# Optimization experiments

Measured on AMD Instinct MI355X. Metric: run time of the kernel, lower is better.

## Reference

```python
import jax, jax.numpy as jnp
import numpy as np

EPS = 1e-8
NEG_FILL = -9e15


def _normalize(x):
    # matches torch cosine_similarity's norm clamp with eps=1e-8
    n = jnp.sqrt(jnp.sum(x * x, axis=-1, keepdims=True))
    return x / jnp.maximum(n, EPS)


def setup_inputs() -> dict:
    key = jax.random.key(0)
    k1, k2 = jax.random.split(key)
    N, D = 8192, 512
    cxr_feats = jax.random.normal(k1, (N, D), dtype=jnp.float32)
    ehr_feats = jax.random.normal(k2, (N, D), dtype=jnp.float32)
    temperature = jnp.asarray(0.07, dtype=jnp.float32)
    return {"cxr_feats": cxr_feats, "ehr_feats": ehr_feats, "temperature": temperature}


def reference(cxr_feats, ehr_feats, temperature):
    # normalize then GEMM instead of broadcasted [N,N,D] cosine_similarity
    cn = _normalize(cxr_feats)                      # [N, D]
    en = _normalize(ehr_feats)                      # [N, D]
    cos_sim = jnp.einsum('id,jd->ij', cn, en)       # [N, N]
    cos_sim = cos_sim / temperature
    N = cos_sim.shape[0]
    eye = jnp.eye(N, dtype=bool)
    diag = jnp.diagonal(cos_sim)                    # positives
    cos_neg = jnp.where(eye, NEG_FILL, cos_sim)     # mask self-pairs
    nll_1 = diag - jax.nn.logsumexp(cos_neg, axis=1)
    nll_2 = diag - jax.nn.logsumexp(cos_neg, axis=0)
    loss = -jnp.mean(nll_1 + nll_2)
    return loss
```

## Files before the change

### kernel.cpp

```cpp
#include <hip/hip_runtime.h>
#include <hip/hip_bf16.h>
#include <stdint.h>
#include <stddef.h>

#define NROWS 8192
#define DDIM  512
#define TILE  128
#define BK    64
#define NBLK  (NROWS / TILE)

static_assert(NBLK == 64, "bj extraction assumes 64 col-blocks");

typedef short bf16x8 __attribute__((ext_vector_type(8)));
typedef float f32x4  __attribute__((ext_vector_type(4)));

__device__ __forceinline__ void async_copy16(const void* g, void* l) {
    __builtin_amdgcn_global_load_lds(
        (const __attribute__((address_space(1))) uint32_t*)g,
        (__attribute__((address_space(3))) uint32_t*)l,
        16, 0, 0);
}

struct bh4 { __hip_bfloat16 x, y, z, w; };

__global__ __launch_bounds__(256) void prep_kernel(
    const float* __restrict__ CXR, const float* __restrict__ EHR,
    __hip_bfloat16* __restrict__ CN, __hip_bfloat16* __restrict__ EN,
    float* __restrict__ rowsum ,
    float* __restrict__ out)
{
    if (blockIdx.x < 64) {
        rowsum[blockIdx.x * 256 + threadIdx.x] = 0.f;
        if (blockIdx.x == 0 && threadIdx.x == 0) out[0] = 0.f;
    }
    const int half = (blockIdx.x >= 2048);
    const float* X = half ? EHR : CXR;
    __hip_bfloat16* Y = half ? EN : CN;
    const int row  = (blockIdx.x & 2047) * 4 + (threadIdx.x >> 6);
    const int lane = threadIdx.x & 63;
    const float* xr = X + (size_t)row * DDIM;
    float4 v0 = ((const float4*)xr)[lane];
    float4 v1 = ((const float4*)xr)[lane + 64];
    float ss = v0.x*v0.x + v0.y*v0.y + v0.z*v0.z + v0.w*v0.w
             + v1.x*v1.x + v1.y*v1.y + v1.z*v1.z + v1.w*v1.w;
    #pragma unroll
    for (int d = 1; d < 64; d <<= 1) ss += __shfl_xor(ss, d);
    const float sc = 1.0f / fmaxf(sqrtf(ss), 1e-8f);
    __hip_bfloat16* yr = Y + (size_t)row * DDIM;
    bh4 o0 = { __float2bfloat16(v0.x*sc), __float2bfloat16(v0.y*sc),
               __float2bfloat16(v0.z*sc), __float2bfloat16(v0.w*sc) };
    bh4 o1 = { __float2bfloat16(v1.x*sc), __float2bfloat16(v1.y*sc),
               __float2bfloat16(v1.z*sc), __float2bfloat16(v1.w*sc) };
    ((bh4*)yr)[lane]      = o0;
    ((bh4*)yr)[lane + 64] = o1;
}

__global__ __launch_bounds__(256, 2) void gemm_loss_kernel(
    const __hip_bfloat16* __restrict__ A,
    const __hip_bfloat16* __restrict__ B,
    const float* __restrict__ temp_p,
    float* __restrict__ rowsum,
    float* __restrict__ colsum,
    float* __restrict__ diagv)
{
    __shared__ __hip_bfloat16 As[TILE * BK];
    __shared__ __hip_bfloat16 Bs[TILE * BK];

    const int tid  = threadIdx.x;
    const int lane = tid & 63;
    const int wv   = tid >> 6;
    const int wi   = (wv >> 1) * 64;
    const int wj   = (wv & 1) * 64;
    const int lcol = lane & 15;
    const int q    = lane >> 4;

    const int bi = blockIdx.x & (NBLK - 1);
    const int bj = blockIdx.x >> 6;
    const int row0 = bi * TILE;
    const int col0 = bj * TILE;

    const int sr = lane >> 3;
    const int su = (lane & 7) ^ sr;
    const __hip_bfloat16* Ag = A + (size_t)(row0 + wv * 32 + sr) * DDIM + su * 8;
    const __hip_bfloat16* Bg = B + (size_t)(col0 + wv * 32 + sr) * DDIM + su * 8;

    f32x4 acc[4][4] = {};

    for (int k0 = 0; k0 < DDIM; k0 += BK) {
        __syncthreads();
        #pragma unroll
        for (int c = 0; c < 4; ++c) {
            async_copy16(Ag + (size_t)(c * 8) * DDIM + k0, &As[(wv * 32 + c * 8) * BK]);
            async_copy16(Bg + (size_t)(c * 8) * DDIM + k0, &Bs[(wv * 32 + c * 8) * BK]);
        }
        __syncthreads();

        #pragma unroll
        for (int kk = 0; kk < 2; ++kk) {
            bf16x8 af[4], bfr[4];
            const int u = kk * 4 + q;
            #pragma unroll
            for (int mt = 0; mt < 4; ++mt) {
                const int r = wi + mt * 16 + lcol;
                const int s = u ^ (r & 7);
                af[mt] = *(const bf16x8*)&As[r * BK + s * 8];
            }
            #pragma unroll
            for (int nt = 0; nt < 4; ++nt) {
                const int r = wj + nt * 16 + lcol;
                const int s = u ^ (r & 7);
                bfr[nt] = *(const bf16x8*)&Bs[r * BK + s * 8];
            }
            #pragma unroll
            for (int mt = 0; mt < 4; ++mt)
                #pragma unroll
                for (int nt = 0; nt < 4; ++nt)
                    acc[mt][nt] = __builtin_amdgcn_mfma_f32_16x16x32_bf16(
                        af[mt], bfr[nt], acc[mt][nt], 0, 0, 0);
        }
    }

    const float invT = 1.0f / temp_p[0];
    const float M = invT;

    float rs[4][4];
    float cs[4];
    #pragma unroll
    for (int mt = 0; mt < 4; ++mt)
        #pragma unroll
        for (int r = 0; r < 4; ++r) rs[mt][r] = 0.f;
    #pragma unroll
    for (int nt = 0; nt < 4; ++nt) cs[nt] = 0.f;

    #pragma unroll
    for (int mt = 0; mt < 4; ++mt) {
        #pragma unroll
        for (int nt = 0; nt < 4; ++nt) {
            #pragma unroll
            for (int r = 0; r < 4; ++r) {
                const int gi = row0 + wi + mt * 16 + q * 4 + r;
                const int gj = col0 + wj + nt * 16 + lcol;
                const float sv = acc[mt][nt][r] * invT;
                float e;
                if (gi == gj) { diagv[gi] = sv; e = 0.f; }
                else          { e = __expf(sv - M); }
                rs[mt][r] += e;
                cs[nt]    += e;
            }
        }
    }

    #pragma unroll
    for (int d = 1; d < 16; d <<= 1)
        #pragma unroll
        for (int mt = 0; mt < 4; ++mt)
            #pragma unroll
            for (int r = 0; r < 4; ++r)
                rs[mt][r] += __shfl_xor(rs[mt][r], d);

    #pragma unroll
    for (int d = 16; d < 64; d <<= 1)
        #pragma unroll
        for (int nt = 0; nt < 4; ++nt)
            cs[nt] += __shfl_xor(cs[nt], d);

    if (lcol == 0) {
        #pragma unroll
        for (int mt = 0; mt < 4; ++mt)
            #pragma unroll
            for (int r = 0; r < 4; ++r)
                atomicAdd(&rowsum[row0 + wi + mt * 16 + q * 4 + r], rs[mt][r]);
    }
    if (q == 0) {
        #pragma unroll
        for (int nt = 0; nt < 4; ++nt)
            atomicAdd(&colsum[col0 + wj + nt * 16 + lcol], cs[nt]);
    }
}

__global__ __launch_bounds__(256) void finalize_kernel(
    const float* __restrict__ rowsum, const float* __restrict__ colsum,
    const float* __restrict__ diagv,  const float* __restrict__ temp_p,
    float* __restrict__ out)
{
    __shared__ float red[4];
    const float M = 1.0f / temp_p[0];
    const int i = blockIdx.x * 256 + threadIdx.x;
    float s = 2.f * M + logf(rowsum[i]) + logf(colsum[i]) - 2.f * diagv[i];
    #pragma unroll
    for (int d = 1; d < 64; d <<= 1) s += __shfl_xor(s, d);
    if ((threadIdx.x & 63) == 0) red[threadIdx.x >> 6] = s;
    __syncthreads();
    if (threadIdx.x == 0)
        atomicAdd(out, (red[0] + red[1] + red[2] + red[3]) / (float)NROWS);
}

extern "C" void kernel_launch(void* const* d_in, const int* in_sizes, int n_in,
                              void* d_out, int out_size, void* d_ws, size_t ws_size,
                              hipStream_t stream) {
    (void)in_sizes; (void)n_in; (void)out_size; (void)ws_size;
    const float* cxr    = (const float*)d_in[0];
    const float* ehr    = (const float*)d_in[1];
    const float* temp_p = (const float*)d_in[2];
    float* out = (float*)d_out;

    float* rowsum = (float*)d_ws;
    float* colsum = rowsum + NROWS;
    float* diagv  = colsum + NROWS;
    __hip_bfloat16* cn = (__hip_bfloat16*)(diagv + NROWS);
    __hip_bfloat16* en = cn + (size_t)NROWS * DDIM;

    prep_kernel<<<4096, 256, 0, stream>>>(cxr, ehr, cn, en, rowsum, out);
    gemm_loss_kernel<<<NBLK * NBLK, 256, 0, stream>>>(cn, en, temp_p, rowsum, colsum, diagv);
    finalize_kernel<<<NROWS / 256, 256, 0, stream>>>(rowsum, colsum, diagv, temp_p, out);
}
```

Before: 164.5 us.

## Switch normalized features to FP8 and use scaled 16x16x128 MFMA

Normalized rows are quantized to FP8 in the prep kernel instead of bf16, and the GEMM uses the MI355X scaled f8f6f4 MFMA with K=128 per instruction. Operand bytes, LDS footprint and MFMA instruction count are all cut, and the occupancy hint rises to 3 blocks per CU. The risk is lower precision of the cosine similarities, which are then scaled by 1/T and exponentiated, so loss accuracy may degrade.

```diff
diff --git a/kernel.cpp b/kernel.cpp
--- a/kernel.cpp
+++ b/kernel.cpp
@@ -6,13 +6,14 @@
 #define NROWS 8192
 #define DDIM  512
 #define TILE  128
-#define BK    64
+#define BKB   128
 #define NBLK  (NROWS / TILE)
 
 static_assert(NBLK == 64, "bj extraction assumes 64 col-blocks");
 
-typedef short bf16x8 __attribute__((ext_vector_type(8)));
-typedef float f32x4  __attribute__((ext_vector_type(4)));
+typedef int   v4i  __attribute__((ext_vector_type(4)));
+typedef int   v8i  __attribute__((ext_vector_type(8)));
+typedef float f32x4 __attribute__((ext_vector_type(4)));
 
 __device__ __forceinline__ void async_copy16(const void* g, void* l) {
     __builtin_amdgcn_global_load_lds(
@@ -21,11 +22,13 @@
         16, 0, 0);
 }
 
-struct bh4 { __hip_bfloat16 x, y, z, w; };
+__device__ __forceinline__ v8i cat8(v4i lo, v4i hi) {
+    return __builtin_shufflevector(lo, hi, 0, 1, 2, 3, 4, 5, 6, 7);
+}
 
 __global__ __launch_bounds__(256) void prep_kernel(
     const float* __restrict__ CXR, const float* __restrict__ EHR,
-    __hip_bfloat16* __restrict__ CN, __hip_bfloat16* __restrict__ EN,
+    uint32_t* __restrict__ CN8, uint32_t* __restrict__ EN8,
     float* __restrict__ rowsum ,
     float* __restrict__ out)
 {
@@ -35,7 +38,7 @@
     }
     const int half = (blockIdx.x >= 2048);
     const float* X = half ? EHR : CXR;
-    __hip_bfloat16* Y = half ? EN : CN;
+    uint32_t* Y = half ? EN8 : CN8;
     const int row  = (blockIdx.x & 2047) * 4 + (threadIdx.x >> 6);
     const int lane = threadIdx.x & 63;
     const float* xr = X + (size_t)row * DDIM;
@@ -46,25 +49,25 @@
     #pragma unroll
     for (int d = 1; d < 64; d <<= 1) ss += __shfl_xor(ss, d);
     const float sc = 1.0f / fmaxf(sqrtf(ss), 1e-8f);
-    __hip_bfloat16* yr = Y + (size_t)row * DDIM;
-    bh4 o0 = { __float2bfloat16(v0.x*sc), __float2bfloat16(v0.y*sc),
-               __float2bfloat16(v0.z*sc), __float2bfloat16(v0.w*sc) };
-    bh4 o1 = { __float2bfloat16(v1.x*sc), __float2bfloat16(v1.y*sc),
-               __float2bfloat16(v1.z*sc), __float2bfloat16(v1.w*sc) };
-    ((bh4*)yr)[lane]      = o0;
-    ((bh4*)yr)[lane + 64] = o1;
-}
-
-__global__ __launch_bounds__(256, 2) void gemm_loss_kernel(
-    const __hip_bfloat16* __restrict__ A,
-    const __hip_bfloat16* __restrict__ B,
+    uint32_t* yr = Y + (size_t)row * (DDIM / 4);
+    int w0 = __builtin_amdgcn_cvt_pk_fp8_f32(v0.x*sc, v0.y*sc, 0, false);
+    w0     = __builtin_amdgcn_cvt_pk_fp8_f32(v0.z*sc, v0.w*sc, w0, true);
+    int w1 = __builtin_amdgcn_cvt_pk_fp8_f32(v1.x*sc, v1.y*sc, 0, false);
+    w1     = __builtin_amdgcn_cvt_pk_fp8_f32(v1.z*sc, v1.w*sc, w1, true);
+    yr[lane]      = (uint32_t)w0;
+    yr[lane + 64] = (uint32_t)w1;
+}
+
+__global__ __launch_bounds__(256, 3) void gemm_loss_kernel(
+    const uint8_t* __restrict__ A,
+    const uint8_t* __restrict__ B,
     const float* __restrict__ temp_p,
     float* __restrict__ rowsum,
     float* __restrict__ colsum,
     float* __restrict__ diagv)
 {
-    __shared__ __hip_bfloat16 As[TILE * BK];
-    __shared__ __hip_bfloat16 Bs[TILE * BK];
+    __shared__ uint8_t As[TILE * BKB];
+    __shared__ uint8_t Bs[TILE * BKB];
 
     const int tid  = threadIdx.x;
     const int lane = tid & 63;
@@ -81,43 +84,46 @@
 
     const int sr = lane >> 3;
     const int su = (lane & 7) ^ sr;
-    const __hip_bfloat16* Ag = A + (size_t)(row0 + wv * 32 + sr) * DDIM + su * 8;
-    const __hip_bfloat16* Bg = B + (size_t)(col0 + wv * 32 + sr) * DDIM + su * 8;
+    const uint8_t* Ag = A + (size_t)(row0 + wv * 32 + sr) * DDIM + su * 16;
+    const uint8_t* Bg = B + (size_t)(col0 + wv * 32 + sr) * DDIM + su * 16;
 
     f32x4 acc[4][4] = {};
 
-    for (int k0 = 0; k0 < DDIM; k0 += BK) {
+    for (int k0 = 0; k0 < DDIM; k0 += BKB) {
         __syncthreads();
         #pragma unroll
         for (int c = 0; c < 4; ++c) {
-            async_copy16(Ag + (size_t)(c * 8) * DDIM + k0, &As[(wv * 32 + c * 8) * BK]);
-            async_copy16(Bg + (size_t)(c * 8) * DDIM + k0, &Bs[(wv * 32 + c * 8) * BK]);
+            async_copy16(Ag + (size_t)(c * 8) * DDIM + k0, &As[(wv * 32 + c * 8) * BKB]);
+            async_copy16(Bg + (size_t)(c * 8) * DDIM + k0, &Bs[(wv * 32 + c * 8) * BKB]);
         }
         __syncthreads();
 
-        #pragma unroll
-        for (int kk = 0; kk < 2; ++kk) {
-            bf16x8 af[4], bfr[4];
-            const int u = kk * 4 + q;
-            #pragma unroll
-            for (int mt = 0; mt < 4; ++mt) {
-                const int r = wi + mt * 16 + lcol;
-                const int s = u ^ (r & 7);
-                af[mt] = *(const bf16x8*)&As[r * BK + s * 8];
-            }
-            #pragma unroll
-            for (int nt = 0; nt < 4; ++nt) {
-                const int r = wj + nt * 16 + lcol;
-                const int s = u ^ (r & 7);
-                bfr[nt] = *(const bf16x8*)&Bs[r * BK + s * 8];
-            }
-            #pragma unroll
-            for (int mt = 0; mt < 4; ++mt)
-                #pragma unroll
-                for (int nt = 0; nt < 4; ++nt)
-                    acc[mt][nt] = __builtin_amdgcn_mfma_f32_16x16x32_bf16(
-                        af[mt], bfr[nt], acc[mt][nt], 0, 0, 0);
-        }
+        v8i af[4], bfr[4];
+        #pragma unroll
+        for (int mt = 0; mt < 4; ++mt) {
+            const int r = wi + mt * 16 + lcol;
+            const int rx = r & 7;
+            v4i lo = *(const v4i*)&As[r * BKB + ((2 * q) ^ rx) * 16];
+            v4i hi = *(const v4i*)&As[r * BKB + ((2 * q + 1) ^ rx) * 16];
+            af[mt] = cat8(lo, hi);
+        }
+        #pragma unroll
+        for (int nt = 0; nt < 4; ++nt) {
+            const int r = wj + nt * 16 + lcol;
+            const int rx = r & 7;
+            v4i lo = *(const v4i*)&Bs[r * BKB + ((2 * q) ^ rx) * 16];
+            v4i hi = *(const v4i*)&Bs[r * BKB + ((2 * q + 1) ^ rx) * 16];
+            bfr[nt] = cat8(lo, hi);
+        }
+        #pragma unroll
+        for (int mt = 0; mt < 4; ++mt)
+            #pragma unroll
+            for (int nt = 0; nt < 4; ++nt)
+                acc[mt][nt] = __builtin_amdgcn_mfma_scale_f32_16x16x128_f8f6f4(
+                    af[mt], bfr[nt], acc[mt][nt],
+                    0 , 0 ,
+                    0, 0x7F7F7F7F,
+                    0, 0x7F7F7F7F);
     }
 
     const float invT = 1.0f / temp_p[0];
@@ -207,10 +213,12 @@
     float* rowsum = (float*)d_ws;
     float* colsum = rowsum + NROWS;
     float* diagv  = colsum + NROWS;
-    __hip_bfloat16* cn = (__hip_bfloat16*)(diagv + NROWS);
-    __hip_bfloat16* en = cn + (size_t)NROWS * DDIM;
-
-    prep_kernel<<<4096, 256, 0, stream>>>(cxr, ehr, cn, en, rowsum, out);
-    gemm_loss_kernel<<<NBLK * NBLK, 256, 0, stream>>>(cn, en, temp_p, rowsum, colsum, diagv);
+    uint32_t* cn8 = (uint32_t*)(diagv + NROWS);
+    uint32_t* en8 = cn8 + (size_t)NROWS * (DDIM / 4);
+    const uint8_t* cnb = (const uint8_t*)cn8;
+    const uint8_t* enb = (const uint8_t*)en8;
+
+    prep_kernel<<<4096, 256, 0, stream>>>(cxr, ehr, cn8, en8, rowsum, out);
+    gemm_loss_kernel<<<NBLK * NBLK, 256, 0, stream>>>(cnb, enb, temp_p, rowsum, colsum, diagv);
     finalize_kernel<<<NROWS / 256, 256, 0, stream>>>(rowsum, colsum, diagv, temp_p, out);
 }
```

After: 386.4 us. +134.9%, slower.
